# Performance work log

Measured on AMD Instinct MI355X. Metric: run time of the kernel, lower is better.

## Reference

```python
import jax, jax.numpy as jnp
import numpy as np

B, N_MAX = 32, 256          # graphs, max nodes per graph (uniform here)
L, D, H, Q, P, F = 4, 256, 8, 4, 16, 32  # layers, hidden, heads, q_dim, pe_dim, phi hidden
NEG = -1e9


def _dense_pos(batch, num_graphs):
    # position of each node inside its (sorted) graph segment
    counts = jax.ops.segment_sum(jnp.ones_like(batch), batch, num_segments=num_graphs)
    starts = jnp.concatenate([jnp.zeros((1,), batch.dtype), jnp.cumsum(counts)[:-1]])
    return jnp.arange(batch.shape[0]) - starts[batch]


def setup_inputs() -> dict:
    key = jax.random.key(0)
    ks = jax.random.split(key, 24)
    N = B * N_MAX
    E = N * 16
    s = 1.0 / np.sqrt(D)
    inp = {
        "x": jax.random.normal(ks[0], (N, D), jnp.float32),
        "z": jax.random.normal(ks[1], (N, Q, P, 2), jnp.float32) * 0.1,
        "Lambda": jax.random.uniform(ks[2], (B, Q, P), jnp.float32),
        "edge_attr": jax.random.normal(ks[3], (E, 16), jnp.float32),
        # attention projections per layer
        "Wq": jax.random.normal(ks[4], (L, D, D), jnp.float32) * s,
        "Wk": jax.random.normal(ks[5], (L, D, D), jnp.float32) * s,
        "Wv": jax.random.normal(ks[6], (L, D, D), jnp.float32) * s,
        "Wo": jax.random.normal(ks[7], (L, D, D), jnp.float32) * s,
        "bq": jnp.zeros((L, D), jnp.float32),
        "bk": jnp.zeros((L, D), jnp.float32),
        "bv": jnp.zeros((L, D), jnp.float32),
        "bo": jnp.zeros((L, D), jnp.float32),
        # eigenvalue MLP (DenseComplexNetwork, SPE-style) per layer
        "phi_W1": jax.random.normal(ks[8], (L, 1, F), jnp.float32),
        "phi_b1": jnp.zeros((L, F), jnp.float32),
        "phi_W2": jax.random.normal(ks[9], (L, F, H), jnp.float32) / np.sqrt(F),
        "phi_b2": jnp.zeros((L, H), jnp.float32),
        # BatchNorm1d affine params per layer
        "bn_gamma": jnp.ones((L, D), jnp.float32),
        "bn_beta": jnp.zeros((L, D), jnp.float32),
        # int inputs
        "edge_index": jax.random.randint(ks[10], (2, E), 0, N),
        "batch": jnp.repeat(jnp.arange(B), N_MAX),
    }
    return inp


def reference(x, z, Lambda, edge_attr, Wq, Wk, Wv, Wo, bq, bk, bv, bo,
              phi_W1, phi_b1, phi_W2, phi_b2, bn_gamma, bn_beta,
              edge_index, batch):
    # edge_index / edge_attr are unused by the original forward as well.
    dh = D // H
    pos = _dense_pos(batch, B)
    mask = jnp.zeros((B, N_MAX), bool).at[batch, pos].set(True)      # [B, n]
    zd = jnp.zeros((B, N_MAX, Q, P, 2), z.dtype).at[batch, pos].set(z)
    zr, zi = zd[..., 0], zd[..., 1]                                   # [B, n, Q, P]

    h0 = x
    for i in range(L):
        # ---- to_dense_batch ----
        hd = jnp.zeros((B, N_MAX, D), x.dtype).at[batch, pos].set(h0)
        # ---- DenseComplexNetwork: phi(Lambda), Re(V diag(phi) V^H) per head ----
        hphi = jax.nn.relu(Lambda[..., None] * phi_W1[i][0] + phi_b1[i])      # [B,Q,P,F]
        phi = jnp.einsum('bqpf,fh->bqph', hphi, phi_W2[i]) + phi_b2[i]        # [B,Q,P,H]
        bias = (jnp.einsum('bqph,biqp,bjqp->bhij', phi, zr, zr)
                + jnp.einsum('bqph,biqp,bjqp->bhij', phi, zi, zi))            # [B,H,n,n]
        # ---- multi-head attention with additive bias + key padding mask ----
        q = (hd @ Wq[i] + bq[i]).reshape(B, N_MAX, H, dh)
        k = (hd @ Wk[i] + bk[i]).reshape(B, N_MAX, H, dh)
        v = (hd @ Wv[i] + bv[i]).reshape(B, N_MAX, H, dh)
        scores = jnp.einsum('bihd,bjhd->bhij', q, k) / jnp.sqrt(jnp.float32(dh)) + bias
        scores = jnp.where(mask[:, None, None, :], scores, NEG)
        attn = jax.nn.softmax(scores, axis=-1)
        o = jnp.einsum('bhij,bjhd->bihd', attn, v).reshape(B, N_MAX, D) @ Wo[i] + bo[i]
        # ---- scatter back (h[mask]), residual, BatchNorm1d (batch stats) ----
        h = o[batch, pos] + h0                                                # [N, D]
        mean = h.mean(axis=0)
        var = ((h - mean) ** 2).mean(axis=0)
        h = (h - mean) / jnp.sqrt(var + 1e-5) * bn_gamma[i] + bn_beta[i]
        h0 = h
    return (h0, z)
```

## Files before the change

### kernel.cpp

```cpp
#include <hip/hip_runtime.h>
#include <hip/hip_bf16.h>

typedef __hip_bfloat16 bf16;
typedef __attribute__((ext_vector_type(8))) short short8v;
typedef __attribute__((ext_vector_type(4))) float f32x4;

constexpr int NB  = 32;
constexpr int NM  = 256;
constexpr int DD  = 256;
constexpr int NH  = 8;
constexpr int QP  = 64;
constexpr int FF  = 32;
constexpr int NT  = NB * NM;
constexpr int HD2 = NT * DD;
constexpr float QSCALE = 0.17677669529663687f;

__device__ __forceinline__ float b2f(unsigned short u) {
  return __uint_as_float(((unsigned)u) << 16);
}
__device__ __forceinline__ short f2b(float f) {
  union { bf16 h; short s; } u;
  u.h = __float2bfloat16(f);
  return u.s;
}

__device__ __forceinline__ void bn_coeffs(const float* bnstat, const float* gamma,
                                          const float* beta, float* bnsc, float* bnsh,
                                          int t) {
  if (t < 256) {
    float sc = 1.f, sh = 0.f;
    if (bnstat) {
      const float mean = bnstat[t] * (1.0f / NT);
      const float var = bnstat[256 + t] * (1.0f / NT) - mean * mean;
      const float rstd = rsqrtf(var + 1e-5f);
      sc = rstd * gamma[t];
      sh = beta[t] - mean * sc;
    }
    bnsc[t] = sc; bnsh[t] = sh;
  }
}

__global__ __launch_bounds__(256) void k_setup(const float* __restrict__ z,
                                               float* __restrict__ outz,
                                               short* __restrict__ zbf,
                                               float* __restrict__ bna,
                                               const float* __restrict__ Lam,
                                               const float* __restrict__ pW1,
                                               const float* __restrict__ pb1,
                                               const float* __restrict__ pW2,
                                               const float* __restrict__ pb2,
                                               float* __restrict__ phiA,
                                               const float* __restrict__ Wq,
                                               const float* __restrict__ Wk,
                                               const float* __restrict__ Wv,
                                               const float* __restrict__ Wo,
                                               short* __restrict__ Wt) {
  __shared__ float Ts[32][33];
  const int t = threadIdx.x;
  const int idx = blockIdx.x * 256 + t;
  {
    const float4 v = ((const float4*)z)[idx];
    ((float4*)outz)[idx] = v;
    short4 s;
    s.x = f2b(v.x); s.y = f2b(v.y); s.z = f2b(v.z); s.w = f2b(v.w);
    ((short4*)zbf)[idx] = s;
  }
  if (idx < 4 * 512) bna[idx] = 0.f;
  if (idx < 4 * 2048) {
    const int l = idx >> 11;
    const int t2 = idx & 2047;
    const int b = t2 >> 6, qp = t2 & 63;
    const float lam = Lam[b * QP + qp];
    const float* w1 = pW1 + l * FF;
    const float* bb1 = pb1 + l * FF;
    const float* w2 = pW2 + l * FF * NH;
    const float* bb2 = pb2 + l * NH;
    float acc[NH];
#pragma unroll
    for (int h = 0; h < NH; ++h) acc[h] = bb2[h];
    for (int f = 0; f < FF; ++f) {
      float a = lam * w1[f] + bb1[f];
      a = a > 0.f ? a : 0.f;
#pragma unroll
      for (int h = 0; h < NH; ++h) acc[h] += a * w2[f * NH + h];
    }
#pragma unroll
    for (int h = 0; h < NH; ++h)
      phiA[(((size_t)l * NB + b) * NH + h) * QP + qp] = acc[h];
  }
  if (blockIdx.x < 128) {
    const int mat = blockIdx.x >> 3;
    const int l = mat >> 2, wsel = mat & 3;
    const float* W = (wsel == 0 ? Wq : wsel == 1 ? Wk : wsel == 2 ? Wv : Wo) + l * DD * DD;
    const int j0 = (blockIdx.x & 7) * 32;
    short* outw = Wt + (size_t)mat * DD * DD;
    const int jj = t & 31, kk8 = t >> 5;
    for (int k0 = 0; k0 < DD; k0 += 32) {
      __syncthreads();
#pragma unroll
      for (int s = 0; s < 4; ++s) {
        const int kl = s * 8 + kk8;
        Ts[kl][jj] = W[(k0 + kl) * DD + j0 + jj];
      }
      __syncthreads();
#pragma unroll
      for (int s = 0; s < 4; ++s) {
        const int jl = (t >> 5) + s * 8;
        const int kl = t & 31;
        outw[(size_t)(j0 + jl) * DD + k0 + kl] = f2b(Ts[kl][jl]);
      }
    }
  }
}

__global__ __launch_bounds__(256) void k_proj(const float* __restrict__ hsrc,
                                              const short* __restrict__ WtL,
                                              const float* __restrict__ bnstat,
                                              const float* __restrict__ gamma,
                                              const float* __restrict__ beta,
                                              const float* __restrict__ b0,
                                              const float* __restrict__ b1,
                                              const float* __restrict__ b2,
                                              short* __restrict__ o0,
                                              short* __restrict__ o1,
                                              short* __restrict__ o2) {
  __shared__ __align__(16) short As[128 * 128];
  __shared__ __align__(16) short Bs[128 * 128];
  __shared__ float bnsc[256], bnsh[256];
  const int t = threadIdx.x;
  const int m0 = blockIdx.x * 128;
  const int j0 = blockIdx.y * 128;
  const int zz = blockIdx.z;
  const short* W = WtL + (size_t)zz * DD * DD;
  const float* bb = zz == 0 ? b0 : zz == 1 ? b1 : b2;
  short* obf = zz == 0 ? o0 : zz == 1 ? o1 : o2;
  const float scale = (zz == 0) ? QSCALE : 1.0f;

  bn_coeffs(bnstat, gamma, beta, bnsc, bnsh, t);

  const int lane = t & 63, w = t >> 6;
  const int wr = w >> 1, wc = w & 1;
  const int fr = lane & 15, fq = lane >> 4;

  f32x4 acc[4][4] = {};

  for (int kb = 0; kb < 2; ++kb) {
    __syncthreads();
#pragma unroll
    for (int p = 0; p < 8; ++p) {
      const int c = p * 256 + t;
      const int r = c >> 4, ch = c & 15;
      const int sw = ((ch ^ (r & 7)) << 4);
      const int col0 = kb * 128 + ch * 8;
      const float* src = hsrc + (size_t)(m0 + r) * 256 + col0;
      const float4 v0 = *(const float4*)src;
      const float4 v1 = *(const float4*)(src + 4);
      short8v o;
      o[0] = f2b(v0.x * bnsc[col0 + 0] + bnsh[col0 + 0]);
      o[1] = f2b(v0.y * bnsc[col0 + 1] + bnsh[col0 + 1]);
      o[2] = f2b(v0.z * bnsc[col0 + 2] + bnsh[col0 + 2]);
      o[3] = f2b(v0.w * bnsc[col0 + 3] + bnsh[col0 + 3]);
      o[4] = f2b(v1.x * bnsc[col0 + 4] + bnsh[col0 + 4]);
      o[5] = f2b(v1.y * bnsc[col0 + 5] + bnsh[col0 + 5]);
      o[6] = f2b(v1.z * bnsc[col0 + 6] + bnsh[col0 + 6]);
      o[7] = f2b(v1.w * bnsc[col0 + 7] + bnsh[col0 + 7]);
      *(short8v*)((char*)As + r * 256 + sw) = o;
      *(short8v*)((char*)Bs + r * 256 + sw) =
          *(const short8v*)(W + (size_t)(j0 + r) * 256 + kb * 128 + ch * 8);
    }
    __syncthreads();
#pragma unroll
    for (int ks = 0; ks < 4; ++ks) {
      short8v a[4], bfrag[4];
#pragma unroll
      for (int m = 0; m < 4; ++m) {
        const int rA = wr * 64 + m * 16 + fr;
        a[m] = *(const short8v*)((const char*)As + rA * 256 + (((ks * 4 + fq) ^ (rA & 7)) << 4));
        const int rB = wc * 64 + m * 16 + fr;
        bfrag[m] = *(const short8v*)((const char*)Bs + rB * 256 + (((ks * 4 + fq) ^ (rB & 7)) << 4));
      }
#pragma unroll
      for (int m = 0; m < 4; ++m)
#pragma unroll
        for (int n = 0; n < 4; ++n)
          acc[m][n] = __builtin_amdgcn_mfma_f32_16x16x32_bf16(a[m], bfrag[n], acc[m][n], 0, 0, 0);
    }
  }
#pragma unroll
  for (int n = 0; n < 4; ++n) {
    const int col = j0 + wc * 64 + n * 16 + fr;
    const float bv = bb[col];
#pragma unroll
    for (int m = 0; m < 4; ++m) {
#pragma unroll
      for (int rr = 0; rr < 4; ++rr) {
        const int row = m0 + wr * 64 + m * 16 + fq * 4 + rr;
        obf[(size_t)row * 256 + col] = f2b((acc[m][n][rr] + bv) * scale);
      }
    }
  }
}

__global__ __launch_bounds__(256) void k_projo(const short* __restrict__ Abf,
                                               const short* __restrict__ WtO,
                                               const float* __restrict__ bo,
                                               const float* __restrict__ hin,
                                               float* __restrict__ hout,
                                               const float* __restrict__ bnstat,
                                               const float* __restrict__ gamma,
                                               const float* __restrict__ beta,
                                               float* __restrict__ bna) {
  __shared__ __align__(16) short As[64 * 128];
  __shared__ __align__(16) short Bs[128 * 128];
  __shared__ float sred[2][128][2];
  __shared__ float bnsc[256], bnsh[256];
  const int t = threadIdx.x;
  const int m0 = blockIdx.x * 64;
  const int c0 = blockIdx.y * 128;
  const int lane = t & 63, w = t >> 6;
  const int wr = w >> 1, wc = w & 1;
  const int fr = lane & 15, fq = lane >> 4;

  bn_coeffs(bnstat, gamma, beta, bnsc, bnsh, t);

  f32x4 acc[2][4] = {};
  for (int kb = 0; kb < 2; ++kb) {
    __syncthreads();
#pragma unroll
    for (int p = 0; p < 4; ++p) {
      const int c = p * 256 + t;
      const int r = c >> 4, ch = c & 15;
      const int sw = ((ch ^ (r & 7)) << 4);
      *(short8v*)((char*)As + r * 256 + sw) =
          *(const short8v*)(Abf + (size_t)(m0 + r) * 256 + kb * 128 + ch * 8);
    }
#pragma unroll
    for (int p = 0; p < 8; ++p) {
      const int c = p * 256 + t;
      const int r = c >> 4, ch = c & 15;
      const int sw = ((ch ^ (r & 7)) << 4);
      *(short8v*)((char*)Bs + r * 256 + sw) =
          *(const short8v*)(WtO + (size_t)(c0 + r) * 256 + kb * 128 + ch * 8);
    }
    __syncthreads();
#pragma unroll
    for (int ks = 0; ks < 4; ++ks) {
      short8v a[2], bfrag[4];
#pragma unroll
      for (int m = 0; m < 2; ++m) {
        const int rA = wr * 32 + m * 16 + fr;
        a[m] = *(const short8v*)((const char*)As + rA * 256 + (((ks * 4 + fq) ^ (rA & 7)) << 4));
      }
#pragma unroll
      for (int n = 0; n < 4; ++n) {
        const int rB = wc * 64 + n * 16 + fr;
        bfrag[n] = *(const short8v*)((const char*)Bs + rB * 256 + (((ks * 4 + fq) ^ (rB & 7)) << 4));
      }
#pragma unroll
      for (int m = 0; m < 2; ++m)
#pragma unroll
        for (int n = 0; n < 4; ++n)
          acc[m][n] = __builtin_amdgcn_mfma_f32_16x16x32_bf16(a[m], bfrag[n], acc[m][n], 0, 0, 0);
    }
  }
#pragma unroll
  for (int n = 0; n < 4; ++n) {
    const int col = c0 + wc * 64 + n * 16 + fr;
    const float bv = bo[col];
    const float sc = bnsc[col], sh = bnsh[col];
    float s = 0.f, ss = 0.f;
#pragma unroll
    for (int m = 0; m < 2; ++m)
#pragma unroll
      for (int rr = 0; rr < 4; ++rr) {
        const int row = m0 + wr * 32 + m * 16 + fq * 4 + rr;
        const size_t idx = (size_t)row * 256 + col;
        const float v = acc[m][n][rr] + bv + (hin[idx] * sc + sh);
        hout[idx] = v;
        s += v;
        ss += v * v;
      }
    s += __shfl_xor(s, 16); s += __shfl_xor(s, 32);
    ss += __shfl_xor(ss, 16); ss += __shfl_xor(ss, 32);
    if (fq == 0) {
      sred[wr][wc * 64 + n * 16 + fr][0] = s;
      sred[wr][wc * 64 + n * 16 + fr][1] = ss;
    }
  }
  __syncthreads();
  if (t < 128) {
    const float s = sred[0][t][0] + sred[1][t][0];
    const float ss = sred[0][t][1] + sred[1][t][1];
    atomicAdd(&bna[c0 + t], s);
    atomicAdd(&bna[256 + c0 + t], ss);
  }
}

__global__ __launch_bounds__(512, 2) void k_attn2(const short* __restrict__ qbf,
                                                  const short* __restrict__ kbf,
                                                  const short* __restrict__ vbf,
                                                  const short* __restrict__ zbf,
                                                  const float* __restrict__ phiAll,
                                                  short* __restrict__ obf, int l) {
  __shared__ __align__(16) char Ks[256 * 384];
  __shared__ __align__(16) char Vt[32 * 512];
  __shared__ __align__(16) char Pw[8 * 2 * 2560];
  __shared__ float rs_l[8 * 32];
  __shared__ float ph2[128];
  const int t = threadIdx.x;
  const int bh = (blockIdx.x & 7) * 32 + (blockIdx.x >> 3);
  const int b = bh >> 3, hh = bh & 7;
  const int bnode = b * 256;

  if (t < 128)
    ph2[t] = phiAll[(((size_t)l * NB + b) * NH + hh) * QP + (t >> 1)];
  __syncthreads();
  {
    const int r = t >> 1, half = t & 1;
    const size_t rowbase = (size_t)(bnode + r) * 256 + hh * 32;
#pragma unroll
    for (int j2 = 0; j2 < 2; ++j2) {
      const int c = half * 2 + j2;
      short8v v = *(const short8v*)(kbf + rowbase + c * 8);
      *(short8v*)(Ks + r * 384 + ((c ^ (r & 7)) << 4)) = v;
    }
    const short* zrow = zbf + (size_t)(bnode + r) * 128 + half * 64;
#pragma unroll
    for (int cc = 0; cc < 8; ++cc) {
      const short8v zv = *(const short8v*)(zrow + cc * 8);
      const int zc = half * 64 + cc * 8;
      short8v o;
#pragma unroll
      for (int e = 0; e < 8; ++e)
        o[e] = f2b(b2f((unsigned short)zv[e]) * ph2[zc + e]);
      const int c = 4 + half * 8 + cc;
      *(short8v*)(Ks + r * 384 + ((c ^ (r & 7)) << 4)) = o;
    }
    const short* vrow = vbf + rowbase + half * 16;
    short8v v0 = *(const short8v*)(vrow);
    short8v v1 = *(const short8v*)(vrow + 8);
#pragma unroll
    for (int dd = 0; dd < 16; ++dd) {
      const int d = half * 16 + dd;
      const short val = dd < 8 ? v0[dd] : v1[dd - 8];
      *(short*)(Vt + d * 512 + (((r >> 3) ^ (d & 7)) << 4) + (r & 7) * 2) = val;
    }
  }
  __syncthreads();

  const int lane = t & 63, w = t >> 6;
  const int fr = lane & 15, fq = lane >> 4;
  const int i0w = w * 32;

  short8v Qf[2][5];
#pragma unroll
  for (int s = 0; s < 2; ++s) {
    const int node = bnode + i0w + s * 16 + fr;
    Qf[s][0] = *(const short8v*)(qbf + (size_t)node * 256 + hh * 32 + fq * 8);
    const short* zr = zbf + (size_t)node * 128;
#pragma unroll
    for (int ks = 1; ks < 5; ++ks)
      Qf[s][ks] = *(const short8v*)(zr + (ks - 1) * 32 + fq * 8);
  }

  f32x4 acc[2][16] = {};
#pragma unroll
  for (int ks = 0; ks < 5; ++ks) {
#pragma unroll
    for (int jt = 0; jt < 16; ++jt) {
      const int row = jt * 16 + fr;
      const short8v a = *(const short8v*)(Ks + row * 384 + (((ks * 4 + fq) ^ (row & 7)) << 4));
      acc[0][jt] = __builtin_amdgcn_mfma_f32_16x16x32_bf16(a, Qf[0][ks], acc[0][jt], 0, 0, 0);
      acc[1][jt] = __builtin_amdgcn_mfma_f32_16x16x32_bf16(a, Qf[1][ks], acc[1][jt], 0, 0, 0);
    }
  }

  float rsv0, rsv1;
#pragma unroll
  for (int s = 0; s < 2; ++s) {
    float m = -1e30f;
#pragma unroll
    for (int jt = 0; jt < 16; ++jt)
#pragma unroll
      for (int rr = 0; rr < 4; ++rr) m = fmaxf(m, acc[s][jt][rr]);
    m = fmaxf(m, __shfl_xor(m, 16));
    m = fmaxf(m, __shfl_xor(m, 32));
    float sm = 0.f;
#pragma unroll
    for (int jt = 0; jt < 16; ++jt)
#pragma unroll
      for (int rr = 0; rr < 4; ++rr) {
        const float e = __expf(acc[s][jt][rr] - m);
        acc[s][jt][rr] = e;
        sm += e;
      }
    sm += __shfl_xor(sm, 16);
    sm += __shfl_xor(sm, 32);
    const float r = 1.0f / sm;
    if (s == 0) rsv0 = r; else rsv1 = r;
  }
  if (fq == 0) rs_l[w * 32 + fr] = rsv0;
  if (fq == 1) rs_l[w * 32 + 16 + fr] = rsv1;

  f32x4 oac[2][2] = {};
  char* pw0 = Pw + w * 5120;
#pragma unroll
  for (int ks = 0; ks < 8; ++ks) {
    char* pw = pw0 + (ks & 1) * 2560;
#pragma unroll
    for (int s = 0; s < 2; ++s)
#pragma unroll
      for (int j2 = 0; j2 < 2; ++j2) {
        const int jt = ks * 2 + j2;
        short4 pk;
        pk.x = f2b(acc[s][jt][0]); pk.y = f2b(acc[s][jt][1]);
        pk.z = f2b(acc[s][jt][2]); pk.w = f2b(acc[s][jt][3]);
        *(short4*)(pw + (s * 16 + fr) * 80 + j2 * 32 + fq * 8) = pk;
      }
    asm volatile("s_waitcnt lgkmcnt(0)" ::: "memory");
    __builtin_amdgcn_sched_barrier(0);
    const short8v pa0 = *(const short8v*)(pw + fr * 80 + fq * 16);
    const short8v pa1 = *(const short8v*)(pw + (16 + fr) * 80 + fq * 16);
    const int sw = (((ks * 4 + fq) ^ (fr & 7)) << 4);
    const short8v vb0 = *(const short8v*)(Vt + fr * 512 + sw);
    const short8v vb1 = *(const short8v*)(Vt + (16 + fr) * 512 + sw);
    oac[0][0] = __builtin_amdgcn_mfma_f32_16x16x32_bf16(pa0, vb0, oac[0][0], 0, 0, 0);
    oac[0][1] = __builtin_amdgcn_mfma_f32_16x16x32_bf16(pa0, vb1, oac[0][1], 0, 0, 0);
    oac[1][0] = __builtin_amdgcn_mfma_f32_16x16x32_bf16(pa1, vb0, oac[1][0], 0, 0, 0);
    oac[1][1] = __builtin_amdgcn_mfma_f32_16x16x32_bf16(pa1, vb1, oac[1][1], 0, 0, 0);
  }

#pragma unroll
  for (int s = 0; s < 2; ++s)
#pragma unroll
    for (int rr = 0; rr < 4; ++rr) {
      const float rs = rs_l[w * 32 + s * 16 + fq * 4 + rr];
      const int node = bnode + i0w + s * 16 + fq * 4 + rr;
#pragma unroll
      for (int nt = 0; nt < 2; ++nt)
        obf[(size_t)node * 256 + hh * 32 + nt * 16 + fr] = f2b(oac[s][nt][rr] * rs);
    }
}

__global__ __launch_bounds__(256) void k_bn_apply(const float* __restrict__ h,
                                                  const float* __restrict__ accum,
                                                  const float* __restrict__ gamma,
                                                  const float* __restrict__ beta,
                                                  float* __restrict__ outp, int l) {
  const int i4 = blockIdx.x * 256 + threadIdx.x;
  const int c0 = (i4 << 2) & 255;
  const float4 v = ((const float4*)h)[i4];
  float vv[4] = {v.x, v.y, v.z, v.w};
  float o[4];
#pragma unroll
  for (int e = 0; e < 4; ++e) {
    const int col = c0 + e;
    const float mean = accum[col] * (1.0f / NT);
    const float var = accum[DD + col] * (1.0f / NT) - mean * mean;
    o[e] = (vv[e] - mean) * rsqrtf(var + 1e-5f) * gamma[l * DD + col] + beta[l * DD + col];
  }
  ((float4*)outp)[i4] = make_float4(o[0], o[1], o[2], o[3]);
}

extern "C" void kernel_launch(void* const* d_in, const int* in_sizes, int n_in,
                              void* d_out, int out_size, void* d_ws, size_t ws_size,
                              hipStream_t stream) {
  (void)in_sizes; (void)n_in; (void)out_size; (void)ws_size;
  const float* x    = (const float*)d_in[0];
  const float* z    = (const float*)d_in[1];
  const float* Lam  = (const float*)d_in[2];
  const float* Wq   = (const float*)d_in[4];
  const float* Wk   = (const float*)d_in[5];
  const float* Wv   = (const float*)d_in[6];
  const float* Wo   = (const float*)d_in[7];
  const float* bq   = (const float*)d_in[8];
  const float* bk   = (const float*)d_in[9];
  const float* bv   = (const float*)d_in[10];
  const float* bo   = (const float*)d_in[11];
  const float* pW1  = (const float*)d_in[12];
  const float* pb1  = (const float*)d_in[13];
  const float* pW2  = (const float*)d_in[14];
  const float* pb2  = (const float*)d_in[15];
  const float* gam  = (const float*)d_in[16];
  const float* bet  = (const float*)d_in[17];
  float* out = (float*)d_out;

  float* h    = (float*)d_ws;
  short* qbf  = (short*)(h + HD2);
  short* kbf  = qbf + HD2;
  short* vbf  = kbf + HD2;
  short* obf  = vbf + HD2;
  short* zbf  = obf + HD2;
  short* Wt   = zbf + NT * 128;
  float* phiA = (float*)(Wt + 16 * DD * DD);
  float* bna  = phiA + 4 * NB * NH * QP;

  k_setup<<<1024, 256, 0, stream>>>(z, out + HD2, zbf, bna, Lam, pW1, pb1, pW2, pb2,
                                    phiA, Wq, Wk, Wv, Wo, Wt);
  for (int l = 0; l < 4; ++l) {
    const float* bnprev = l ? bna + (l - 1) * 512 : nullptr;
    const float* gprev  = gam + (l ? (l - 1) * DD : 0);
    const float* bprev  = bet + (l ? (l - 1) * DD : 0);
    const float* hsrc   = l ? h : x;
    k_proj<<<dim3(64, 2, 3), 256, 0, stream>>>(hsrc, Wt + (size_t)l * 4 * DD * DD,
                                               bnprev, gprev, bprev,
                                               bq + l * DD, bk + l * DD, bv + l * DD,
                                               qbf, kbf, vbf);
    k_attn2<<<256, 512, 0, stream>>>(qbf, kbf, vbf, zbf, phiA, obf, l);
    k_projo<<<dim3(128, 2), 256, 0, stream>>>(obf, Wt + (size_t)(l * 4 + 3) * DD * DD,
                                              bo + l * DD, hsrc, h,
                                              bnprev, gprev, bprev, bna + l * 512);
  }
  k_bn_apply<<<2048, 256, 0, stream>>>(h, bna + 3 * 512, gam, bet, out, 3);
}
```

Before: 157.9 us.

## Halve attention block to 4 waves, each handling 64 query rows

The attention kernel now launches 256 threads (4 waves) per (graph, head) block instead of 512, and each wave processes 64 query rows instead of 32. Each K/bias fragment read from LDS is reused across four MFMAs instead of two, and the staging loop gives each thread a whole row. This cuts LDS read traffic per MFMA and the per-wave setup cost. In exchange, register pressure roughly doubles (acc[4][16] is 256 floats), which risks spills or low occupancy, and there are fewer waves available to hide latency.

```diff
diff --git a/kernel.cpp b/kernel.cpp
--- a/kernel.cpp
+++ b/kernel.cpp
@@ -296,7 +296,7 @@
   }
 }
 
-__global__ __launch_bounds__(512, 2) void k_attn2(const short* __restrict__ qbf,
+__global__ __launch_bounds__(256, 1) void k_attn2(const short* __restrict__ qbf,
                                                   const short* __restrict__ kbf,
                                                   const short* __restrict__ vbf,
                                                   const short* __restrict__ zbf,
@@ -304,8 +304,8 @@
                                                   short* __restrict__ obf, int l) {
   __shared__ __align__(16) char Ks[256 * 384];
   __shared__ __align__(16) char Vt[32 * 512];
-  __shared__ __align__(16) char Pw[8 * 2 * 2560];
-  __shared__ float rs_l[8 * 32];
+  __shared__ __align__(16) char Pw[4 * 2 * 5120];
+  __shared__ float rs_l[256];
   __shared__ float ph2[128];
   const int t = threadIdx.x;
   const int bh = (blockIdx.x & 7) * 32 + (blockIdx.x >> 3);
@@ -316,33 +316,33 @@
     ph2[t] = phiAll[(((size_t)l * NB + b) * NH + hh) * QP + (t >> 1)];
   __syncthreads();
   {
-    const int r = t >> 1, half = t & 1;
+    const int r = t;
     const size_t rowbase = (size_t)(bnode + r) * 256 + hh * 32;
 #pragma unroll
-    for (int j2 = 0; j2 < 2; ++j2) {
-      const int c = half * 2 + j2;
+    for (int c = 0; c < 4; ++c) {
       short8v v = *(const short8v*)(kbf + rowbase + c * 8);
       *(short8v*)(Ks + r * 384 + ((c ^ (r & 7)) << 4)) = v;
     }
-    const short* zrow = zbf + (size_t)(bnode + r) * 128 + half * 64;
-#pragma unroll
-    for (int cc = 0; cc < 8; ++cc) {
+    const short* zrow = zbf + (size_t)(bnode + r) * 128;
+#pragma unroll
+    for (int cc = 0; cc < 16; ++cc) {
       const short8v zv = *(const short8v*)(zrow + cc * 8);
-      const int zc = half * 64 + cc * 8;
+      const int zc = cc * 8;
       short8v o;
 #pragma unroll
       for (int e = 0; e < 8; ++e)
         o[e] = f2b(b2f((unsigned short)zv[e]) * ph2[zc + e]);
-      const int c = 4 + half * 8 + cc;
+      const int c = 4 + cc;
       *(short8v*)(Ks + r * 384 + ((c ^ (r & 7)) << 4)) = o;
     }
-    const short* vrow = vbf + rowbase + half * 16;
+    const short* vrow = vbf + rowbase;
     short8v v0 = *(const short8v*)(vrow);
     short8v v1 = *(const short8v*)(vrow + 8);
-#pragma unroll
-    for (int dd = 0; dd < 16; ++dd) {
-      const int d = half * 16 + dd;
-      const short val = dd < 8 ? v0[dd] : v1[dd - 8];
+    short8v v2 = *(const short8v*)(vrow + 16);
+    short8v v3 = *(const short8v*)(vrow + 24);
+#pragma unroll
+    for (int d = 0; d < 32; ++d) {
+      const short val = d < 8 ? v0[d] : d < 16 ? v1[d - 8] : d < 24 ? v2[d - 16] : v3[d - 24];
       *(short*)(Vt + d * 512 + (((r >> 3) ^ (d & 7)) << 4) + (r & 7) * 2) = val;
     }
   }
@@ -350,11 +350,11 @@
 
   const int lane = t & 63, w = t >> 6;
   const int fr = lane & 15, fq = lane >> 4;
-  const int i0w = w * 32;
-
-  short8v Qf[2][5];
-#pragma unroll
-  for (int s = 0; s < 2; ++s) {
+  const int i0w = w * 64;
+
+  short8v Qf[4][5];
+#pragma unroll
+  for (int s = 0; s < 4; ++s) {
     const int node = bnode + i0w + s * 16 + fr;
     Qf[s][0] = *(const short8v*)(qbf + (size_t)node * 256 + hh * 32 + fq * 8);
     const short* zr = zbf + (size_t)node * 128;
@@ -363,21 +363,21 @@
       Qf[s][ks] = *(const short8v*)(zr + (ks - 1) * 32 + fq * 8);
   }
 
-  f32x4 acc[2][16] = {};
+  f32x4 acc[4][16] = {};
 #pragma unroll
   for (int ks = 0; ks < 5; ++ks) {
 #pragma unroll
     for (int jt = 0; jt < 16; ++jt) {
       const int row = jt * 16 + fr;
       const short8v a = *(const short8v*)(Ks + row * 384 + (((ks * 4 + fq) ^ (row & 7)) << 4));
-      acc[0][jt] = __builtin_amdgcn_mfma_f32_16x16x32_bf16(a, Qf[0][ks], acc[0][jt], 0, 0, 0);
-      acc[1][jt] = __builtin_amdgcn_mfma_f32_16x16x32_bf16(a, Qf[1][ks], acc[1][jt], 0, 0, 0);
-    }
-  }
-
-  float rsv0, rsv1;
-#pragma unroll
-  for (int s = 0; s < 2; ++s) {
+#pragma unroll
+      for (int s = 0; s < 4; ++s)
+        acc[s][jt] = __builtin_amdgcn_mfma_f32_16x16x32_bf16(a, Qf[s][ks], acc[s][jt], 0, 0, 0);
+    }
+  }
+
+#pragma unroll
+  for (int s = 0; s < 4; ++s) {
     float m = -1e30f;
 #pragma unroll
     for (int jt = 0; jt < 16; ++jt)
@@ -396,19 +396,16 @@
       }
     sm += __shfl_xor(sm, 16);
     sm += __shfl_xor(sm, 32);
-    const float r = 1.0f / sm;
-    if (s == 0) rsv0 = r; else rsv1 = r;
-  }
-  if (fq == 0) rs_l[w * 32 + fr] = rsv0;
-  if (fq == 1) rs_l[w * 32 + 16 + fr] = rsv1;
-
-  f32x4 oac[2][2] = {};
-  char* pw0 = Pw + w * 5120;
+    if (fq == s) rs_l[w * 64 + s * 16 + fr] = 1.0f / sm;
+  }
+
+  f32x4 oac[4][2] = {};
+  char* pw0 = Pw + w * 10240;
 #pragma unroll
   for (int ks = 0; ks < 8; ++ks) {
-    char* pw = pw0 + (ks & 1) * 2560;
-#pragma unroll
-    for (int s = 0; s < 2; ++s)
+    char* pw = pw0 + (ks & 1) * 5120;
+#pragma unroll
+    for (int s = 0; s < 4; ++s)
 #pragma unroll
       for (int j2 = 0; j2 < 2; ++j2) {
         const int jt = ks * 2 + j2;
@@ -419,22 +416,22 @@
       }
     asm volatile("s_waitcnt lgkmcnt(0)" ::: "memory");
     __builtin_amdgcn_sched_barrier(0);
-    const short8v pa0 = *(const short8v*)(pw + fr * 80 + fq * 16);
-    const short8v pa1 = *(const short8v*)(pw + (16 + fr) * 80 + fq * 16);
     const int sw = (((ks * 4 + fq) ^ (fr & 7)) << 4);
     const short8v vb0 = *(const short8v*)(Vt + fr * 512 + sw);
     const short8v vb1 = *(const short8v*)(Vt + (16 + fr) * 512 + sw);
-    oac[0][0] = __builtin_amdgcn_mfma_f32_16x16x32_bf16(pa0, vb0, oac[0][0], 0, 0, 0);
-    oac[0][1] = __builtin_amdgcn_mfma_f32_16x16x32_bf16(pa0, vb1, oac[0][1], 0, 0, 0);
-    oac[1][0] = __builtin_amdgcn_mfma_f32_16x16x32_bf16(pa1, vb0, oac[1][0], 0, 0, 0);
-    oac[1][1] = __builtin_amdgcn_mfma_f32_16x16x32_bf16(pa1, vb1, oac[1][1], 0, 0, 0);
-  }
-
-#pragma unroll
-  for (int s = 0; s < 2; ++s)
+#pragma unroll
+    for (int s = 0; s < 4; ++s) {
+      const short8v pa = *(const short8v*)(pw + (s * 16 + fr) * 80 + fq * 16);
+      oac[s][0] = __builtin_amdgcn_mfma_f32_16x16x32_bf16(pa, vb0, oac[s][0], 0, 0, 0);
+      oac[s][1] = __builtin_amdgcn_mfma_f32_16x16x32_bf16(pa, vb1, oac[s][1], 0, 0, 0);
+    }
+  }
+
+#pragma unroll
+  for (int s = 0; s < 4; ++s)
 #pragma unroll
     for (int rr = 0; rr < 4; ++rr) {
-      const float rs = rs_l[w * 32 + s * 16 + fq * 4 + rr];
+      const float rs = rs_l[w * 64 + s * 16 + fq * 4 + rr];
       const int node = bnode + i0w + s * 16 + fq * 4 + rr;
 #pragma unroll
       for (int nt = 0; nt < 2; ++nt)
@@ -506,7 +503,7 @@
                                                bnprev, gprev, bprev,
                                                bq + l * DD, bk + l * DD, bv + l * DD,
                                                qbf, kbf, vbf);
-    k_attn2<<<256, 512, 0, stream>>>(qbf, kbf, vbf, zbf, phiA, obf, l);
+    k_attn2<<<256, 256, 0, stream>>>(qbf, kbf, vbf, zbf, phiA, obf, l);
     k_projo<<<dim3(128, 2), 256, 0, stream>>>(obf, Wt + (size_t)(l * 4 + 3) * DD * DD,
                                               bo + l * DD, hsrc, h,
                                               bnprev, gprev, bprev, bna + l * 512);
```

After: 183.7 us. +16.3%, slower.

## Fuse QKV projection into per-(graph, head) attention kernel

Applied to the files above, without the earlier changes.

Replaces the separate k_proj GEMM and k_attn2 kernels with one k_fat kernel. Each block first normalizes its graph's 256 node rows, then computes that head's 96 Q/K/V columns with MFMA and writes K and transposed V straight into LDS. Q is staged in a per-warp scratch area, which removes the bf16 Q/K/V global write and read and one launch per layer. In exchange, each graph's h rows are reloaded and BN-converted once per head, eight times in total. The kernel also uses about 156 KB of shared memory, which limits occupancy to one block per CU.

```diff
diff --git a/kernel.cpp b/kernel.cpp
--- a/kernel.cpp
+++ b/kernel.cpp
@@ -113,46 +113,49 @@
   }
 }
 
-__global__ __launch_bounds__(256) void k_proj(const float* __restrict__ hsrc,
-                                              const short* __restrict__ WtL,
-                                              const float* __restrict__ bnstat,
-                                              const float* __restrict__ gamma,
-                                              const float* __restrict__ beta,
-                                              const float* __restrict__ b0,
-                                              const float* __restrict__ b1,
-                                              const float* __restrict__ b2,
-                                              short* __restrict__ o0,
-                                              short* __restrict__ o1,
-                                              short* __restrict__ o2) {
-  __shared__ __align__(16) short As[128 * 128];
-  __shared__ __align__(16) short Bs[128 * 128];
-  __shared__ float bnsc[256], bnsh[256];
+__global__ __launch_bounds__(512, 2) void k_fat(const float* __restrict__ hsrc,
+                                                const short* __restrict__ WtL,
+                                                const float* __restrict__ bnstat,
+                                                const float* __restrict__ gamma,
+                                                const float* __restrict__ beta,
+                                                const float* __restrict__ bq_l,
+                                                const float* __restrict__ bk_l,
+                                                const float* __restrict__ bv_l,
+                                                const short* __restrict__ zbf,
+                                                const float* __restrict__ phiAll,
+                                                short* __restrict__ obf, int l) {
+  __shared__ __align__(16) char SM[159232];
+  char* Ks = SM;
+  char* Hs = SM;
+  char* Ws = SM + 65536;
+  char* Vt = SM + 98304;
+  char* Pw = SM + 114688;
+  float* rs_l = (float*)(SM + 155648);
+  float* ph2  = (float*)(SM + 156672);
+  float* bnsc = (float*)(SM + 157184);
+  float* bnsh = bnsc + 256;
+
   const int t = threadIdx.x;
-  const int m0 = blockIdx.x * 128;
-  const int j0 = blockIdx.y * 128;
-  const int zz = blockIdx.z;
-  const short* W = WtL + (size_t)zz * DD * DD;
-  const float* bb = zz == 0 ? b0 : zz == 1 ? b1 : b2;
-  short* obf = zz == 0 ? o0 : zz == 1 ? o1 : o2;
-  const float scale = (zz == 0) ? QSCALE : 1.0f;
+  const int bh = (blockIdx.x & 7) * 32 + (blockIdx.x >> 3);
+  const int b = bh >> 3, hh = bh & 7;
+  const int bnode = b * 256;
 
   bn_coeffs(bnstat, gamma, beta, bnsc, bnsh, t);
+  if (t < 128)
+    ph2[t] = phiAll[(((size_t)l * NB + b) * NH + hh) * QP + (t >> 1)];
 
   const int lane = t & 63, w = t >> 6;
-  const int wr = w >> 1, wc = w & 1;
   const int fr = lane & 15, fq = lane >> 4;
 
-  f32x4 acc[4][4] = {};
-
+  f32x4 pacc[2][6] = {};
   for (int kb = 0; kb < 2; ++kb) {
     __syncthreads();
 #pragma unroll
     for (int p = 0; p < 8; ++p) {
-      const int c = p * 256 + t;
+      const int c = p * 512 + t;
       const int r = c >> 4, ch = c & 15;
-      const int sw = ((ch ^ (r & 7)) << 4);
       const int col0 = kb * 128 + ch * 8;
-      const float* src = hsrc + (size_t)(m0 + r) * 256 + col0;
+      const float* src = hsrc + (size_t)(bnode + r) * 256 + col0;
       const float4 v0 = *(const float4*)src;
       const float4 v1 = *(const float4*)(src + 4);
       short8v o;
@@ -164,41 +167,168 @@
       o[5] = f2b(v1.y * bnsc[col0 + 5] + bnsh[col0 + 5]);
       o[6] = f2b(v1.z * bnsc[col0 + 6] + bnsh[col0 + 6]);
       o[7] = f2b(v1.w * bnsc[col0 + 7] + bnsh[col0 + 7]);
-      *(short8v*)((char*)As + r * 256 + sw) = o;
-      *(short8v*)((char*)Bs + r * 256 + sw) =
-          *(const short8v*)(W + (size_t)(j0 + r) * 256 + kb * 128 + ch * 8);
+      *(short8v*)(Hs + r * 256 + ((ch ^ (r & 7)) << 4)) = o;
+    }
+#pragma unroll
+    for (int p = 0; p < 3; ++p) {
+      const int c = p * 512 + t;
+      const int r = c >> 4, ch = c & 15;
+      const int mat = r >> 5, jj = r & 31;
+      *(short8v*)(Ws + r * 256 + ((ch ^ (r & 7)) << 4)) =
+          *(const short8v*)(WtL + ((size_t)mat * 256 + hh * 32 + jj) * 256 + kb * 128 + ch * 8);
     }
     __syncthreads();
 #pragma unroll
     for (int ks = 0; ks < 4; ++ks) {
-      short8v a[4], bfrag[4];
-#pragma unroll
-      for (int m = 0; m < 4; ++m) {
-        const int rA = wr * 64 + m * 16 + fr;
-        a[m] = *(const short8v*)((const char*)As + rA * 256 + (((ks * 4 + fq) ^ (rA & 7)) << 4));
-        const int rB = wc * 64 + m * 16 + fr;
-        bfrag[m] = *(const short8v*)((const char*)Bs + rB * 256 + (((ks * 4 + fq) ^ (rB & 7)) << 4));
-      }
-#pragma unroll
-      for (int m = 0; m < 4; ++m)
-#pragma unroll
-        for (int n = 0; n < 4; ++n)
-          acc[m][n] = __builtin_amdgcn_mfma_f32_16x16x32_bf16(a[m], bfrag[n], acc[m][n], 0, 0, 0);
-    }
-  }
-#pragma unroll
-  for (int n = 0; n < 4; ++n) {
-    const int col = j0 + wc * 64 + n * 16 + fr;
-    const float bv = bb[col];
-#pragma unroll
-    for (int m = 0; m < 4; ++m) {
+      short8v a[2], bfr[6];
+#pragma unroll
+      for (int m = 0; m < 2; ++m) {
+        const int rA = w * 32 + m * 16 + fr;
+        a[m] = *(const short8v*)(Hs + rA * 256 + (((ks * 4 + fq) ^ (rA & 7)) << 4));
+      }
+#pragma unroll
+      for (int n = 0; n < 6; ++n) {
+        const int rB = n * 16 + fr;
+        bfr[n] = *(const short8v*)(Ws + rB * 256 + (((ks * 4 + fq) ^ (rB & 7)) << 4));
+      }
+#pragma unroll
+      for (int m = 0; m < 2; ++m)
+#pragma unroll
+        for (int n = 0; n < 6; ++n)
+          pacc[m][n] = __builtin_amdgcn_mfma_f32_16x16x32_bf16(a[m], bfr[n], pacc[m][n], 0, 0, 0);
+    }
+  }
+  __syncthreads();
+
+  char* qtmp = Pw + w * 5120;
+  {
+    const float* bqp = bq_l + hh * 32;
+    const float* bkp = bk_l + hh * 32;
+    const float* bvp = bv_l + hh * 32;
+#pragma unroll
+    for (int m = 0; m < 2; ++m) {
 #pragma unroll
       for (int rr = 0; rr < 4; ++rr) {
-        const int row = m0 + wr * 64 + m * 16 + fq * 4 + rr;
-        obf[(size_t)row * 256 + col] = f2b((acc[m][n][rr] + bv) * scale);
-      }
-    }
-  }
+        const int nodel = m * 16 + fq * 4 + rr;
+        const int node = w * 32 + nodel;
+#pragma unroll
+        for (int n2 = 0; n2 < 2; ++n2) {
+          const int col = n2 * 16 + fr;
+          *(short*)(qtmp + nodel * 80 + col * 2) =
+              f2b((pacc[m][n2][rr] + bqp[col]) * QSCALE);
+          *(short*)(Ks + node * 384 + (((col >> 3) ^ (node & 7)) << 4) + (col & 7) * 2) =
+              f2b(pacc[m][n2 + 2][rr] + bkp[col]);
+          *(short*)(Vt + col * 512 + (((node >> 3) ^ (col & 7)) << 4) + (node & 7) * 2) =
+              f2b(pacc[m][n2 + 4][rr] + bvp[col]);
+        }
+      }
+    }
+  }
+  {
+    const int r = t >> 1, half = t & 1;
+    const short* zrow = zbf + (size_t)(bnode + r) * 128 + half * 64;
+#pragma unroll
+    for (int cc = 0; cc < 8; ++cc) {
+      const short8v zv = *(const short8v*)(zrow + cc * 8);
+      const int zc = half * 64 + cc * 8;
+      short8v o;
+#pragma unroll
+      for (int e = 0; e < 8; ++e)
+        o[e] = f2b(b2f((unsigned short)zv[e]) * ph2[zc + e]);
+      const int c = 4 + half * 8 + cc;
+      *(short8v*)(Ks + r * 384 + ((c ^ (r & 7)) << 4)) = o;
+    }
+  }
+  __syncthreads();
+
+  const int i0w = w * 32;
+  short8v Qf[2][5];
+#pragma unroll
+  for (int s = 0; s < 2; ++s) {
+    Qf[s][0] = *(const short8v*)(qtmp + (s * 16 + fr) * 80 + fq * 16);
+    const short* zr = zbf + (size_t)(bnode + i0w + s * 16 + fr) * 128;
+#pragma unroll
+    for (int ks = 1; ks < 5; ++ks)
+      Qf[s][ks] = *(const short8v*)(zr + (ks - 1) * 32 + fq * 8);
+  }
+
+  f32x4 acc[2][16] = {};
+#pragma unroll
+  for (int ks = 0; ks < 5; ++ks) {
+#pragma unroll
+    for (int jt = 0; jt < 16; ++jt) {
+      const int row = jt * 16 + fr;
+      const short8v a = *(const short8v*)(Ks + row * 384 + (((ks * 4 + fq) ^ (row & 7)) << 4));
+      acc[0][jt] = __builtin_amdgcn_mfma_f32_16x16x32_bf16(a, Qf[0][ks], acc[0][jt], 0, 0, 0);
+      acc[1][jt] = __builtin_amdgcn_mfma_f32_16x16x32_bf16(a, Qf[1][ks], acc[1][jt], 0, 0, 0);
+    }
+  }
+
+  float rsv0, rsv1;
+#pragma unroll
+  for (int s = 0; s < 2; ++s) {
+    float m = -1e30f;
+#pragma unroll
+    for (int jt = 0; jt < 16; ++jt)
+#pragma unroll
+      for (int rr = 0; rr < 4; ++rr) m = fmaxf(m, acc[s][jt][rr]);
+    m = fmaxf(m, __shfl_xor(m, 16));
+    m = fmaxf(m, __shfl_xor(m, 32));
+    float sm = 0.f;
+#pragma unroll
+    for (int jt = 0; jt < 16; ++jt)
+#pragma unroll
+      for (int rr = 0; rr < 4; ++rr) {
+        const float e = __expf(acc[s][jt][rr] - m);
+        acc[s][jt][rr] = e;
+        sm += e;
+      }
+    sm += __shfl_xor(sm, 16);
+    sm += __shfl_xor(sm, 32);
+    const float r = 1.0f / sm;
+    if (s == 0) rsv0 = r; else rsv1 = r;
+  }
+  if (fq == 0) rs_l[w * 32 + fr] = rsv0;
+  if (fq == 1) rs_l[w * 32 + 16 + fr] = rsv1;
+
+  f32x4 oac[2][2] = {};
+  char* pw0 = Pw + w * 5120;
+#pragma unroll
+  for (int ks = 0; ks < 8; ++ks) {
+    char* pw = pw0 + (ks & 1) * 2560;
+#pragma unroll
+    for (int s = 0; s < 2; ++s)
+#pragma unroll
+      for (int j2 = 0; j2 < 2; ++j2) {
+        const int jt = ks * 2 + j2;
+        short4 pk;
+        pk.x = f2b(acc[s][jt][0]); pk.y = f2b(acc[s][jt][1]);
+        pk.z = f2b(acc[s][jt][2]); pk.w = f2b(acc[s][jt][3]);
+        *(short4*)(pw + (s * 16 + fr) * 80 + j2 * 32 + fq * 8) = pk;
+      }
+    asm volatile("s_waitcnt lgkmcnt(0)" ::: "memory");
+    __builtin_amdgcn_sched_barrier(0);
+    const short8v pa0 = *(const short8v*)(pw + fr * 80 + fq * 16);
+    const short8v pa1 = *(const short8v*)(pw + (16 + fr) * 80 + fq * 16);
+    const int sw = (((ks * 4 + fq) ^ (fr & 7)) << 4);
+    const short8v vb0 = *(const short8v*)(Vt + fr * 512 + sw);
+    const short8v vb1 = *(const short8v*)(Vt + (16 + fr) * 512 + sw);
+    oac[0][0] = __builtin_amdgcn_mfma_f32_16x16x32_bf16(pa0, vb0, oac[0][0], 0, 0, 0);
+    oac[0][1] = __builtin_amdgcn_mfma_f32_16x16x32_bf16(pa0, vb1, oac[0][1], 0, 0, 0);
+    oac[1][0] = __builtin_amdgcn_mfma_f32_16x16x32_bf16(pa1, vb0, oac[1][0], 0, 0, 0);
+    oac[1][1] = __builtin_amdgcn_mfma_f32_16x16x32_bf16(pa1, vb1, oac[1][1], 0, 0, 0);
+  }
+
+#pragma unroll
+  for (int s = 0; s < 2; ++s)
+#pragma unroll
+    for (int rr = 0; rr < 4; ++rr) {
+      const float rs = rs_l[w * 32 + s * 16 + fq * 4 + rr];
+      const int node = bnode + i0w + s * 16 + fq * 4 + rr;
+#pragma unroll
+      for (int nt = 0; nt < 2; ++nt)
+        obf[(size_t)node * 256 + hh * 32 + nt * 16 + fr] = f2b(oac[s][nt][rr] * rs);
+    }
 }
 
 __global__ __launch_bounds__(256) void k_projo(const short* __restrict__ Abf,
@@ -294,152 +424,6 @@
     atomicAdd(&bna[c0 + t], s);
     atomicAdd(&bna[256 + c0 + t], ss);
   }
-}
-
-__global__ __launch_bounds__(512, 2) void k_attn2(const short* __restrict__ qbf,
-                                                  const short* __restrict__ kbf,
-                                                  const short* __restrict__ vbf,
-                                                  const short* __restrict__ zbf,
-                                                  const float* __restrict__ phiAll,
-                                                  short* __restrict__ obf, int l) {
-  __shared__ __align__(16) char Ks[256 * 384];
-  __shared__ __align__(16) char Vt[32 * 512];
-  __shared__ __align__(16) char Pw[8 * 2 * 2560];
-  __shared__ float rs_l[8 * 32];
-  __shared__ float ph2[128];
-  const int t = threadIdx.x;
-  const int bh = (blockIdx.x & 7) * 32 + (blockIdx.x >> 3);
-  const int b = bh >> 3, hh = bh & 7;
-  const int bnode = b * 256;
-
-  if (t < 128)
-    ph2[t] = phiAll[(((size_t)l * NB + b) * NH + hh) * QP + (t >> 1)];
-  __syncthreads();
-  {
-    const int r = t >> 1, half = t & 1;
-    const size_t rowbase = (size_t)(bnode + r) * 256 + hh * 32;
-#pragma unroll
-    for (int j2 = 0; j2 < 2; ++j2) {
-      const int c = half * 2 + j2;
-      short8v v = *(const short8v*)(kbf + rowbase + c * 8);
-      *(short8v*)(Ks + r * 384 + ((c ^ (r & 7)) << 4)) = v;
-    }
-    const short* zrow = zbf + (size_t)(bnode + r) * 128 + half * 64;
-#pragma unroll
-    for (int cc = 0; cc < 8; ++cc) {
-      const short8v zv = *(const short8v*)(zrow + cc * 8);
-      const int zc = half * 64 + cc * 8;
-      short8v o;
-#pragma unroll
-      for (int e = 0; e < 8; ++e)
-        o[e] = f2b(b2f((unsigned short)zv[e]) * ph2[zc + e]);
-      const int c = 4 + half * 8 + cc;
-      *(short8v*)(Ks + r * 384 + ((c ^ (r & 7)) << 4)) = o;
-    }
-    const short* vrow = vbf + rowbase + half * 16;
-    short8v v0 = *(const short8v*)(vrow);
-    short8v v1 = *(const short8v*)(vrow + 8);
-#pragma unroll
-    for (int dd = 0; dd < 16; ++dd) {
-      const int d = half * 16 + dd;
-      const short val = dd < 8 ? v0[dd] : v1[dd - 8];
-      *(short*)(Vt + d * 512 + (((r >> 3) ^ (d & 7)) << 4) + (r & 7) * 2) = val;
-    }
-  }
-  __syncthreads();
-
-  const int lane = t & 63, w = t >> 6;
-  const int fr = lane & 15, fq = lane >> 4;
-  const int i0w = w * 32;
-
-  short8v Qf[2][5];
-#pragma unroll
-  for (int s = 0; s < 2; ++s) {
-    const int node = bnode + i0w + s * 16 + fr;
-    Qf[s][0] = *(const short8v*)(qbf + (size_t)node * 256 + hh * 32 + fq * 8);
-    const short* zr = zbf + (size_t)node * 128;
-#pragma unroll
-    for (int ks = 1; ks < 5; ++ks)
-      Qf[s][ks] = *(const short8v*)(zr + (ks - 1) * 32 + fq * 8);
-  }
-
-  f32x4 acc[2][16] = {};
-#pragma unroll
-  for (int ks = 0; ks < 5; ++ks) {
-#pragma unroll
-    for (int jt = 0; jt < 16; ++jt) {
-      const int row = jt * 16 + fr;
-      const short8v a = *(const short8v*)(Ks + row * 384 + (((ks * 4 + fq) ^ (row & 7)) << 4));
-      acc[0][jt] = __builtin_amdgcn_mfma_f32_16x16x32_bf16(a, Qf[0][ks], acc[0][jt], 0, 0, 0);
-      acc[1][jt] = __builtin_amdgcn_mfma_f32_16x16x32_bf16(a, Qf[1][ks], acc[1][jt], 0, 0, 0);
-    }
-  }
-
-  float rsv0, rsv1;
-#pragma unroll
-  for (int s = 0; s < 2; ++s) {
-    float m = -1e30f;
-#pragma unroll
-    for (int jt = 0; jt < 16; ++jt)
-#pragma unroll
-      for (int rr = 0; rr < 4; ++rr) m = fmaxf(m, acc[s][jt][rr]);
-    m = fmaxf(m, __shfl_xor(m, 16));
-    m = fmaxf(m, __shfl_xor(m, 32));
-    float sm = 0.f;
-#pragma unroll
-    for (int jt = 0; jt < 16; ++jt)
-#pragma unroll
-      for (int rr = 0; rr < 4; ++rr) {
-        const float e = __expf(acc[s][jt][rr] - m);
-        acc[s][jt][rr] = e;
-        sm += e;
-      }
-    sm += __shfl_xor(sm, 16);
-    sm += __shfl_xor(sm, 32);
-    const float r = 1.0f / sm;
-    if (s == 0) rsv0 = r; else rsv1 = r;
-  }
-  if (fq == 0) rs_l[w * 32 + fr] = rsv0;
-  if (fq == 1) rs_l[w * 32 + 16 + fr] = rsv1;
-
-  f32x4 oac[2][2] = {};
-  char* pw0 = Pw + w * 5120;
-#pragma unroll
-  for (int ks = 0; ks < 8; ++ks) {
-    char* pw = pw0 + (ks & 1) * 2560;
-#pragma unroll
-    for (int s = 0; s < 2; ++s)
-#pragma unroll
-      for (int j2 = 0; j2 < 2; ++j2) {
-        const int jt = ks * 2 + j2;
-        short4 pk;
-        pk.x = f2b(acc[s][jt][0]); pk.y = f2b(acc[s][jt][1]);
-        pk.z = f2b(acc[s][jt][2]); pk.w = f2b(acc[s][jt][3]);
-        *(short4*)(pw + (s * 16 + fr) * 80 + j2 * 32 + fq * 8) = pk;
-      }
-    asm volatile("s_waitcnt lgkmcnt(0)" ::: "memory");
-    __builtin_amdgcn_sched_barrier(0);
-    const short8v pa0 = *(const short8v*)(pw + fr * 80 + fq * 16);
-    const short8v pa1 = *(const short8v*)(pw + (16 + fr) * 80 + fq * 16);
-    const int sw = (((ks * 4 + fq) ^ (fr & 7)) << 4);
-    const short8v vb0 = *(const short8v*)(Vt + fr * 512 + sw);
-    const short8v vb1 = *(const short8v*)(Vt + (16 + fr) * 512 + sw);
-    oac[0][0] = __builtin_amdgcn_mfma_f32_16x16x32_bf16(pa0, vb0, oac[0][0], 0, 0, 0);
-    oac[0][1] = __builtin_amdgcn_mfma_f32_16x16x32_bf16(pa0, vb1, oac[0][1], 0, 0, 0);
-    oac[1][0] = __builtin_amdgcn_mfma_f32_16x16x32_bf16(pa1, vb0, oac[1][0], 0, 0, 0);
-    oac[1][1] = __builtin_amdgcn_mfma_f32_16x16x32_bf16(pa1, vb1, oac[1][1], 0, 0, 0);
-  }
-
-#pragma unroll
-  for (int s = 0; s < 2; ++s)
-#pragma unroll
-    for (int rr = 0; rr < 4; ++rr) {
-      const float rs = rs_l[w * 32 + s * 16 + fq * 4 + rr];
-      const int node = bnode + i0w + s * 16 + fq * 4 + rr;
-#pragma unroll
-      for (int nt = 0; nt < 2; ++nt)
-        obf[(size_t)node * 256 + hh * 32 + nt * 16 + fr] = f2b(oac[s][nt][rr] * rs);
-    }
 }
 
 __global__ __launch_bounds__(256) void k_bn_apply(const float* __restrict__ h,
@@ -486,10 +470,7 @@
   float* out = (float*)d_out;
 
   float* h    = (float*)d_ws;
-  short* qbf  = (short*)(h + HD2);
-  short* kbf  = qbf + HD2;
-  short* vbf  = kbf + HD2;
-  short* obf  = vbf + HD2;
+  short* obf  = (short*)(h + HD2);
   short* zbf  = obf + HD2;
   short* Wt   = zbf + NT * 128;
   float* phiA = (float*)(Wt + 16 * DD * DD);
@@ -502,11 +483,10 @@
     const float* gprev  = gam + (l ? (l - 1) * DD : 0);
     const float* bprev  = bet + (l ? (l - 1) * DD : 0);
     const float* hsrc   = l ? h : x;
-    k_proj<<<dim3(64, 2, 3), 256, 0, stream>>>(hsrc, Wt + (size_t)l * 4 * DD * DD,
-                                               bnprev, gprev, bprev,
-                                               bq + l * DD, bk + l * DD, bv + l * DD,
-                                               qbf, kbf, vbf);
-    k_attn2<<<256, 512, 0, stream>>>(qbf, kbf, vbf, zbf, phiA, obf, l);
+    k_fat<<<256, 512, 0, stream>>>(hsrc, Wt + (size_t)l * 4 * DD * DD,
+                                   bnprev, gprev, bprev,
+                                   bq + l * DD, bk + l * DD, bv + l * DD,
+                                   zbf, phiA, obf, l);
     k_projo<<<dim3(128, 2), 256, 0, stream>>>(obf, Wt + (size_t)(l * 4 + 3) * DD * DD,
                                               bo + l * DD, hsrc, h,
                                               bnprev, gprev, bprev, bna + l * 512);
```

Result: faster. 141.7 us (-10.3%).
